# Kernel tuning notes

Measured on AMD Instinct MI355X. Metric: run time of the kernel, lower is better.

## Reference

```python
import jax, jax.numpy as jnp
import numpy as np

B, S, K, F = 256, 512, 32, 64
H1, H2 = 512, 256


def setup_inputs() -> dict:
    key = jax.random.key(0)
    ks = jax.random.split(key, 8)
    x = jax.random.normal(ks[0], (B, S, F), dtype=jnp.float32)
    neighborhood = jax.random.randint(ks[1], (S, K), 0, S)
    distances = jax.random.uniform(ks[2], (S, K), dtype=jnp.float32)
    in_w = K * (F + 1)  # 2080
    W1 = jax.random.normal(ks[3], (in_w, H1), dtype=jnp.float32) * 0.02
    b1 = jnp.zeros((H1,), dtype=jnp.float32)
    W2 = jax.random.normal(ks[4], (H1, H2), dtype=jnp.float32) * 0.02
    b2 = jnp.zeros((H2,), dtype=jnp.float32)
    Wd = jax.random.normal(ks[5], (H2, 1), dtype=jnp.float32) * 0.02
    bd = jnp.zeros((1,), dtype=jnp.float32)
    return {"x": x, "neighborhood": neighborhood, "distances": distances,
            "W1": W1, "b1": b1, "W2": W2, "b2": b2, "Wd": Wd, "bd": bd}


def reference(x, neighborhood, distances, W1, b1, W2, b2, Wd, bd):
    b, s, f = x.shape
    k = neighborhood.shape[1]
    # make_k_tensor: gather neighbors and append per-edge distance
    gathered = x[:, neighborhood, :]                      # [B, S, K, F]
    dist = jnp.broadcast_to(distances[None, :, :, None], (b, s, k, 1))
    kt = jnp.concatenate([gathered, dist], axis=-1)        # [B, S, K, F+1]
    # filter phase: shared MLP over flattened neighborhoods
    flat = kt.reshape(b * s, k * (f + 1))                  # [B*S, K*(F+1)]
    h = jax.nn.relu(flat @ W1 + b1)
    h = h @ W2 + b2                                        # [B*S, H2]
    h = h.reshape(b, s, -1)
    # max pool over sequence, then final dense
    m = jnp.max(h, axis=1)                                 # [B, H2]
    out = jax.nn.relu(m) @ Wd + bd                         # [B, 1]
    return out.squeeze(1)                                  # [B]
```

## Files before the change

kernel.cpp:

```cpp
#include <hip/hip_runtime.h>

typedef __attribute__((ext_vector_type(8))) short short8;
typedef __attribute__((ext_vector_type(4))) float f32x4;

constexpr int Bb = 256, Ss = 512, Kk = 32, Ff = 64, H1 = 512, H2 = 256;
constexpr int Mtot = Bb * Ss;
constexpr int KD1 = Kk * Ff;

#define DEVI static __device__ __forceinline__

DEVI unsigned short f2b(float f) {
  unsigned u = __float_as_uint(f);
  return (unsigned short)((u + 0x7FFFu + ((u >> 16) & 1u)) >> 16);
}

DEVI void stage16(const void* g, void* l) {
  __builtin_amdgcn_global_load_lds((const __attribute__((address_space(1))) void*)g,
                                   (__attribute__((address_space(3))) void*)l, 16, 0, 0);
}

__global__ void k_cvt_x(const float* __restrict__ x, unsigned short* __restrict__ xbf) {
  int i = blockIdx.x * 256 + threadIdx.x;
  float4 v = ((const float4*)x)[i];
  ushort4 o;
  o.x = f2b(v.x); o.y = f2b(v.y); o.z = f2b(v.z); o.w = f2b(v.w);
  ((ushort4*)xbf)[i] = o;
}

__global__ void k_w1t(const float* __restrict__ W1, unsigned short* __restrict__ w1t) {
  int idx = blockIdx.x * 256 + threadIdx.x;
  int h = idx >> 11, i = idx & 2047;
  int k = i >> 6, f = i & 63;
  w1t[idx] = f2b(W1[(k * 65 + f) * 512 + h]);
}

__global__ void k_w2t(const float* __restrict__ W2, unsigned short* __restrict__ w2t) {
  int idx = blockIdx.x * 256 + threadIdx.x;
  int n = idx >> 9, k = idx & 511;
  w2t[idx] = f2b(W2[k * 256 + n]);
}

__global__ void k_dbias(const float* __restrict__ W1, const float* __restrict__ b1,
                        const float* __restrict__ dist, float* __restrict__ dbias) {
  int idx = blockIdx.x * 256 + threadIdx.x;
  int s = idx >> 9, h = idx & 511;
  float a = b1[h];
  #pragma unroll
  for (int k = 0; k < 32; ++k)
    a += dist[s * 32 + k] * W1[(k * 65 + 64) * 512 + h];
  dbias[idx] = a;
}

__global__ __launch_bounds__(256, 2) void k_gemm1(
    const unsigned short* __restrict__ xbf, const unsigned short* __restrict__ w1t,
    const int* __restrict__ nb, const float* __restrict__ dbias,
    unsigned short* __restrict__ h1) {
  __shared__ __align__(16) unsigned short As[128 * 64];
  __shared__ __align__(16) unsigned short Bs[128 * 64];
  const int tid = threadIdx.x;
  const int lane = tid & 63;
  const int w = tid >> 6;
  const int wm = w >> 1, wn = w & 1;
  const int mblk = blockIdx.x >> 2;
  const int nblk = blockIdx.x & 3;
  const int r0 = mblk << 7;
  const int b = r0 >> 9;
  const int s0 = r0 & 511;
  const int ncol0 = nblk << 7;
  const int arow = lane >> 3;
  const int acol = (lane & 7) << 3;

  f32x4 acc[4][4];
  #pragma unroll
  for (int m = 0; m < 4; ++m)
    #pragma unroll
    for (int n = 0; n < 4; ++n) acc[m][n] = (f32x4){0.f, 0.f, 0.f, 0.f};

  for (int t = 0; t < 32; ++t) {
    #pragma unroll
    for (int i = 0; i < 4; ++i) {
      int rr = (w << 5) + (i << 3);
      int row = rr + arow;
      int j = nb[((s0 + row) << 5) + t];
      stage16(xbf + (((size_t)((b << 9) + j)) << 6) + acol, As + rr * 64);
    }
    #pragma unroll
    for (int i = 0; i < 4; ++i) {
      int rr = (w << 5) + (i << 3);
      int row = rr + arow;
      stage16(w1t + (((size_t)(ncol0 + row)) << 11) + (t << 6) + acol, Bs + rr * 64);
    }
    __syncthreads();
    #pragma unroll
    for (int ks = 0; ks < 2; ++ks) {
      short8 af[4], bfr[4];
      #pragma unroll
      for (int m = 0; m < 4; ++m)
        af[m] = *(const short8*)(As + ((wm << 6) + (m << 4) + (lane & 15)) * 64 + (ks << 5) + ((lane >> 4) << 3));
      #pragma unroll
      for (int n = 0; n < 4; ++n)
        bfr[n] = *(const short8*)(Bs + ((wn << 6) + (n << 4) + (lane & 15)) * 64 + (ks << 5) + ((lane >> 4) << 3));
      #pragma unroll
      for (int m = 0; m < 4; ++m)
        #pragma unroll
        for (int n = 0; n < 4; ++n)
          acc[m][n] = __builtin_amdgcn_mfma_f32_16x16x32_bf16(af[m], bfr[n], acc[m][n], 0, 0, 0);
    }
    __syncthreads();
  }

  #pragma unroll
  for (int m = 0; m < 4; ++m) {
    int rowl = (wm << 6) + (m << 4) + ((lane >> 4) << 2);
    #pragma unroll
    for (int n = 0; n < 4; ++n) {
      int col = ncol0 + (wn << 6) + (n << 4) + (lane & 15);
      #pragma unroll
      for (int r = 0; r < 4; ++r) {
        int row = r0 + rowl + r;
        float v = acc[m][n][r] + dbias[((row & 511) << 9) + col];
        v = v > 0.f ? v : 0.f;
        h1[((size_t)row << 9) + col] = f2b(v);
      }
    }
  }
}

__global__ __launch_bounds__(256, 2) void k_gemm2(
    const unsigned short* __restrict__ h1, const unsigned short* __restrict__ w2t,
    const float* __restrict__ b2, unsigned* __restrict__ mrelu) {
  __shared__ __align__(16) unsigned short As[128 * 64];
  __shared__ __align__(16) unsigned short Bs[128 * 64];
  const int tid = threadIdx.x;
  const int lane = tid & 63;
  const int w = tid >> 6;
  const int wm = w >> 1, wn = w & 1;
  const int mblk = blockIdx.x >> 1;
  const int nblk = blockIdx.x & 1;
  const int r0 = mblk << 7;
  const int b = r0 >> 9;
  const int ncol0 = nblk << 7;
  const int arow = lane >> 3;
  const int acol = (lane & 7) << 3;

  f32x4 acc[4][4];
  #pragma unroll
  for (int m = 0; m < 4; ++m)
    #pragma unroll
    for (int n = 0; n < 4; ++n) acc[m][n] = (f32x4){0.f, 0.f, 0.f, 0.f};

  for (int t = 0; t < 8; ++t) {
    #pragma unroll
    for (int i = 0; i < 4; ++i) {
      int rr = (w << 5) + (i << 3);
      int row = rr + arow;
      stage16(h1 + (((size_t)(r0 + row)) << 9) + (t << 6) + acol, As + rr * 64);
      stage16(w2t + (((size_t)(ncol0 + row)) << 9) + (t << 6) + acol, Bs + rr * 64);
    }
    __syncthreads();
    #pragma unroll
    for (int ks = 0; ks < 2; ++ks) {
      short8 af[4], bfr[4];
      #pragma unroll
      for (int m = 0; m < 4; ++m)
        af[m] = *(const short8*)(As + ((wm << 6) + (m << 4) + (lane & 15)) * 64 + (ks << 5) + ((lane >> 4) << 3));
      #pragma unroll
      for (int n = 0; n < 4; ++n)
        bfr[n] = *(const short8*)(Bs + ((wn << 6) + (n << 4) + (lane & 15)) * 64 + (ks << 5) + ((lane >> 4) << 3));
      #pragma unroll
      for (int m = 0; m < 4; ++m)
        #pragma unroll
        for (int n = 0; n < 4; ++n)
          acc[m][n] = __builtin_amdgcn_mfma_f32_16x16x32_bf16(af[m], bfr[n], acc[m][n], 0, 0, 0);
    }
    __syncthreads();
  }

  #pragma unroll
  for (int n = 0; n < 4; ++n) {
    int col = ncol0 + (wn << 6) + (n << 4) + (lane & 15);
    float cm = -1e30f;
    #pragma unroll
    for (int m = 0; m < 4; ++m)
      #pragma unroll
      for (int r = 0; r < 4; ++r) cm = fmaxf(cm, acc[m][n][r]);
    cm = fmaxf(cm, __shfl_xor(cm, 16));
    cm = fmaxf(cm, __shfl_xor(cm, 32));
    if ((lane >> 4) == 0) {
      float v = fmaxf(cm + b2[col], 0.f);
      atomicMax(mrelu + ((b << 8) + col), __float_as_uint(v));
    }
  }
}

__global__ void k_final(const unsigned* __restrict__ mrelu, const float* __restrict__ wd,
                        const float* __restrict__ bd, float* __restrict__ out) {
  int b = blockIdx.x, t = threadIdx.x;
  float v = __uint_as_float(mrelu[(b << 8) + t]) * wd[t];
  #pragma unroll
  for (int o = 32; o > 0; o >>= 1) v += __shfl_down(v, o);
  __shared__ float p[4];
  if ((t & 63) == 0) p[t >> 6] = v;
  __syncthreads();
  if (t == 0) out[b] = p[0] + p[1] + p[2] + p[3] + bd[0];
}

extern "C" void kernel_launch(void* const* d_in, const int* in_sizes, int n_in,
                              void* d_out, int out_size, void* d_ws, size_t ws_size,
                              hipStream_t stream) {
  (void)in_sizes; (void)n_in; (void)out_size; (void)ws_size;
  const float* x    = (const float*)d_in[0];
  const int*   nb   = (const int*)d_in[1];
  const float* dist = (const float*)d_in[2];
  const float* W1   = (const float*)d_in[3];
  const float* b1   = (const float*)d_in[4];
  const float* W2   = (const float*)d_in[5];
  const float* b2   = (const float*)d_in[6];
  const float* Wd   = (const float*)d_in[7];
  const float* bd   = (const float*)d_in[8];
  float* out = (float*)d_out;

  char* p = (char*)d_ws;
  unsigned short* xbf   = (unsigned short*)p; p += (size_t)Bb * Ss * Ff * 2;
  unsigned short* w1t   = (unsigned short*)p; p += (size_t)H1 * KD1 * 2;
  unsigned short* w2t   = (unsigned short*)p; p += (size_t)H2 * H1 * 2;
  float*          dbias = (float*)p;          p += (size_t)Ss * H1 * 4;
  unsigned*       mrelu = (unsigned*)p;       p += (size_t)Bb * H2 * 4;
  unsigned short* h1    = (unsigned short*)p; p += (size_t)Mtot * H1 * 2;

  hipMemsetAsync(mrelu, 0, (size_t)Bb * H2 * 4, stream);
  k_cvt_x<<<(Bb * Ss * Ff / 4) / 256, 256, 0, stream>>>(x, xbf);
  k_w1t<<<(H1 * KD1) / 256, 256, 0, stream>>>(W1, w1t);
  k_w2t<<<(H2 * H1) / 256, 256, 0, stream>>>(W2, w2t);
  k_dbias<<<(Ss * H1) / 256, 256, 0, stream>>>(W1, b1, dist, dbias);
  k_gemm1<<<(Mtot / 128) * (H1 / 128), 256, 0, stream>>>(xbf, w1t, nb, dbias, h1);
  k_gemm2<<<(Mtot / 128) * (H2 / 128), 256, 0, stream>>>(h1, w2t, b2, mrelu);
  k_final<<<Bb, 256, 0, stream>>>(mrelu, Wd, bd, out);
}
```

Measured before the change: 463.6 us.

## Swizzle LDS tiles and split GEMM chain into halves for L2-resident h1

Applies an XOR swizzle to the global-to-LDS staging column and the matching MFMA fragment reads in both GEMMs, so LDS reads should hit fewer bank conflicts. It adds an explicit vmcnt(0) wait before the barrier so the async LDS loads are complete before use. It also splits the batch rows into two halves, running gemm1 then gemm2 per half with a half-sized h1 buffer. This keeps the intermediate smaller and more likely to stay in cache, at the cost of extra launches and smaller grids per launch.

```diff
diff --git a/kernel.cpp b/kernel.cpp
--- a/kernel.cpp
+++ b/kernel.cpp
@@ -5,6 +5,7 @@
 
 constexpr int Bb = 256, Ss = 512, Kk = 32, Ff = 64, H1 = 512, H2 = 256;
 constexpr int Mtot = Bb * Ss;
+constexpr int Mh = Mtot / 2;
 constexpr int KD1 = Kk * Ff;
 
 #define DEVI static __device__ __forceinline__
@@ -51,10 +52,11 @@
   dbias[idx] = a;
 }
 
+
 __global__ __launch_bounds__(256, 2) void k_gemm1(
     const unsigned short* __restrict__ xbf, const unsigned short* __restrict__ w1t,
     const int* __restrict__ nb, const float* __restrict__ dbias,
-    unsigned short* __restrict__ h1) {
+    unsigned short* __restrict__ h1, int mbase) {
   __shared__ __align__(16) unsigned short As[128 * 64];
   __shared__ __align__(16) unsigned short Bs[128 * 64];
   const int tid = threadIdx.x;
@@ -63,12 +65,13 @@
   const int wm = w >> 1, wn = w & 1;
   const int mblk = blockIdx.x >> 2;
   const int nblk = blockIdx.x & 3;
-  const int r0 = mblk << 7;
-  const int b = r0 >> 9;
-  const int s0 = r0 & 511;
+  const int r0l = mblk << 7;
+  const int r0g = mbase + r0l;
+  const int b = r0g >> 9;
+  const int s0 = r0g & 511;
   const int ncol0 = nblk << 7;
   const int arow = lane >> 3;
-  const int acol = (lane & 7) << 3;
+  const int scol = (((lane & 7) ^ (lane >> 3)) << 3);
 
   f32x4 acc[4][4];
   #pragma unroll
@@ -82,24 +85,26 @@
       int rr = (w << 5) + (i << 3);
       int row = rr + arow;
       int j = nb[((s0 + row) << 5) + t];
-      stage16(xbf + (((size_t)((b << 9) + j)) << 6) + acol, As + rr * 64);
+      stage16(xbf + (((size_t)((b << 9) + j)) << 6) + scol, As + rr * 64);
     }
     #pragma unroll
     for (int i = 0; i < 4; ++i) {
       int rr = (w << 5) + (i << 3);
       int row = rr + arow;
-      stage16(w1t + (((size_t)(ncol0 + row)) << 11) + (t << 6) + acol, Bs + rr * 64);
-    }
+      stage16(w1t + (((size_t)(ncol0 + row)) << 11) + (t << 6) + scol, Bs + rr * 64);
+    }
+    asm volatile("s_waitcnt vmcnt(0)" ::: "memory");
     __syncthreads();
     #pragma unroll
     for (int ks = 0; ks < 2; ++ks) {
+      const int rdoff = ((((ks << 2) + (lane >> 4)) ^ (lane & 7)) << 3);
       short8 af[4], bfr[4];
       #pragma unroll
       for (int m = 0; m < 4; ++m)
-        af[m] = *(const short8*)(As + ((wm << 6) + (m << 4) + (lane & 15)) * 64 + (ks << 5) + ((lane >> 4) << 3));
+        af[m] = *(const short8*)(As + ((wm << 6) + (m << 4) + (lane & 15)) * 64 + rdoff);
       #pragma unroll
       for (int n = 0; n < 4; ++n)
-        bfr[n] = *(const short8*)(Bs + ((wn << 6) + (n << 4) + (lane & 15)) * 64 + (ks << 5) + ((lane >> 4) << 3));
+        bfr[n] = *(const short8*)(Bs + ((wn << 6) + (n << 4) + (lane & 15)) * 64 + rdoff);
       #pragma unroll
       for (int m = 0; m < 4; ++m)
         #pragma unroll
@@ -117,10 +122,10 @@
       int col = ncol0 + (wn << 6) + (n << 4) + (lane & 15);
       #pragma unroll
       for (int r = 0; r < 4; ++r) {
-        int row = r0 + rowl + r;
-        float v = acc[m][n][r] + dbias[((row & 511) << 9) + col];
+        int rowL = r0l + rowl + r;
+        float v = acc[m][n][r] + dbias[(((r0g + rowl + r) & 511) << 9) + col];
         v = v > 0.f ? v : 0.f;
-        h1[((size_t)row << 9) + col] = f2b(v);
+        h1[((size_t)rowL << 9) + col] = f2b(v);
       }
     }
   }
@@ -128,7 +133,7 @@
 
 __global__ __launch_bounds__(256, 2) void k_gemm2(
     const unsigned short* __restrict__ h1, const unsigned short* __restrict__ w2t,
-    const float* __restrict__ b2, unsigned* __restrict__ mrelu) {
+    const float* __restrict__ b2, unsigned* __restrict__ mrelu, int mbase) {
   __shared__ __align__(16) unsigned short As[128 * 64];
   __shared__ __align__(16) unsigned short Bs[128 * 64];
   const int tid = threadIdx.x;
@@ -137,11 +142,11 @@
   const int wm = w >> 1, wn = w & 1;
   const int mblk = blockIdx.x >> 1;
   const int nblk = blockIdx.x & 1;
-  const int r0 = mblk << 7;
-  const int b = r0 >> 9;
+  const int r0l = mblk << 7;
+  const int b = (mbase + r0l) >> 9;
   const int ncol0 = nblk << 7;
   const int arow = lane >> 3;
-  const int acol = (lane & 7) << 3;
+  const int scol = (((lane & 7) ^ (lane >> 3)) << 3);
 
   f32x4 acc[4][4];
   #pragma unroll
@@ -154,19 +159,21 @@
     for (int i = 0; i < 4; ++i) {
       int rr = (w << 5) + (i << 3);
       int row = rr + arow;
-      stage16(h1 + (((size_t)(r0 + row)) << 9) + (t << 6) + acol, As + rr * 64);
-      stage16(w2t + (((size_t)(ncol0 + row)) << 9) + (t << 6) + acol, Bs + rr * 64);
-    }
+      stage16(h1 + (((size_t)(r0l + row)) << 9) + (t << 6) + scol, As + rr * 64);
+      stage16(w2t + (((size_t)(ncol0 + row)) << 9) + (t << 6) + scol, Bs + rr * 64);
+    }
+    asm volatile("s_waitcnt vmcnt(0)" ::: "memory");
     __syncthreads();
     #pragma unroll
     for (int ks = 0; ks < 2; ++ks) {
+      const int rdoff = ((((ks << 2) + (lane >> 4)) ^ (lane & 7)) << 3);
       short8 af[4], bfr[4];
       #pragma unroll
       for (int m = 0; m < 4; ++m)
-        af[m] = *(const short8*)(As + ((wm << 6) + (m << 4) + (lane & 15)) * 64 + (ks << 5) + ((lane >> 4) << 3));
+        af[m] = *(const short8*)(As + ((wm << 6) + (m << 4) + (lane & 15)) * 64 + rdoff);
       #pragma unroll
       for (int n = 0; n < 4; ++n)
-        bfr[n] = *(const short8*)(Bs + ((wn << 6) + (n << 4) + (lane & 15)) * 64 + (ks << 5) + ((lane >> 4) << 3));
+        bfr[n] = *(const short8*)(Bs + ((wn << 6) + (n << 4) + (lane & 15)) * 64 + rdoff);
       #pragma unroll
       for (int m = 0; m < 4; ++m)
         #pragma unroll
@@ -226,14 +233,17 @@
   unsigned short* w2t   = (unsigned short*)p; p += (size_t)H2 * H1 * 2;
   float*          dbias = (float*)p;          p += (size_t)Ss * H1 * 4;
   unsigned*       mrelu = (unsigned*)p;       p += (size_t)Bb * H2 * 4;
-  unsigned short* h1    = (unsigned short*)p; p += (size_t)Mtot * H1 * 2;
+  unsigned short* h1    = (unsigned short*)p; p += (size_t)Mh * H1 * 2;
 
   hipMemsetAsync(mrelu, 0, (size_t)Bb * H2 * 4, stream);
   k_cvt_x<<<(Bb * Ss * Ff / 4) / 256, 256, 0, stream>>>(x, xbf);
   k_w1t<<<(H1 * KD1) / 256, 256, 0, stream>>>(W1, w1t);
   k_w2t<<<(H2 * H1) / 256, 256, 0, stream>>>(W2, w2t);
   k_dbias<<<(Ss * H1) / 256, 256, 0, stream>>>(W1, b1, dist, dbias);
-  k_gemm1<<<(Mtot / 128) * (H1 / 128), 256, 0, stream>>>(xbf, w1t, nb, dbias, h1);
-  k_gemm2<<<(Mtot / 128) * (H2 / 128), 256, 0, stream>>>(h1, w2t, b2, mrelu);
+  for (int hh = 0; hh < 2; ++hh) {
+    int mbase = hh * Mh;
+    k_gemm1<<<(Mh / 128) * (H1 / 128), 256, 0, stream>>>(xbf, w1t, nb, dbias, h1, mbase);
+    k_gemm2<<<(Mh / 128) * (H2 / 128), 256, 0, stream>>>(h1, w2t, b2, mrelu, mbase);
+  }
   k_final<<<Bb, 256, 0, stream>>>(mrelu, Wd, bd, out);
 }
```

Measured after the change: 442.8 us. 4.5% less time.

## Fuse both MLP GEMMs into one kernel keeping h1 in LDS

Applied to the files above, without the earlier changes.

Merges gemm1 and gemm2 into one kernel in which each 512-thread block computes a 128-row by full-512-column h1 tile and keeps it in LDS as bf16, then runs the second GEMM and max-pool from there. This removes the h1 round trip through global memory. The distance feature is folded in as an extra K window (bf16 distances times W1 distance rows) in place of the precomputed fp32 dbias table. The K loop uses a three-slot LDS ring with global_load_lds prefetch, swizzled LDS layouts and raw vmcnt/barrier control. The trade-off is one block per CU with 144KB of LDS, lower occupancy, and bf16 rounding of the distances.

```diff
diff --git a/kernel.cpp b/kernel.cpp
--- a/kernel.cpp
+++ b/kernel.cpp
@@ -4,10 +4,11 @@
 typedef __attribute__((ext_vector_type(4))) float f32x4;
 
 constexpr int Bb = 256, Ss = 512, Kk = 32, Ff = 64, H1 = 512, H2 = 256;
-constexpr int Mtot = Bb * Ss;
-constexpr int KD1 = Kk * Ff;
+constexpr int KD1E = 2080;
 
 #define DEVI static __device__ __forceinline__
+#define BARRIER asm volatile("s_barrier" ::: "memory")
+#define VMCNT(N) asm volatile("s_waitcnt vmcnt(" #N ")" ::: "memory")
 
 DEVI unsigned short f2b(float f) {
   unsigned u = __float_as_uint(f);
@@ -27,11 +28,20 @@
   ((ushort4*)xbf)[i] = o;
 }
 
+__global__ void k_cvt_dist(const float* __restrict__ dist, unsigned short* __restrict__ distbf) {
+  int i = blockIdx.x * 256 + threadIdx.x;
+  float4 v = ((const float4*)dist)[i];
+  ushort4 o;
+  o.x = f2b(v.x); o.y = f2b(v.y); o.z = f2b(v.z); o.w = f2b(v.w);
+  ((ushort4*)distbf)[i] = o;
+}
+
 __global__ void k_w1t(const float* __restrict__ W1, unsigned short* __restrict__ w1t) {
-  int idx = blockIdx.x * 256 + threadIdx.x;
-  int h = idx >> 11, i = idx & 2047;
-  int k = i >> 6, f = i & 63;
-  w1t[idx] = f2b(W1[(k * 65 + f) * 512 + h]);
+  int h = blockIdx.x;
+  for (int k = threadIdx.x; k < KD1E; k += 256) {
+    int row = (k < 2048) ? ((k >> 6) * 65 + (k & 63)) : ((k - 2048) * 65 + 64);
+    w1t[h * KD1E + k] = f2b(W1[row * 512 + h]);
+  }
 }
 
 __global__ void k_w2t(const float* __restrict__ W2, unsigned short* __restrict__ w2t) {
@@ -40,150 +50,145 @@
   w2t[idx] = f2b(W2[k * 256 + n]);
 }
 
-__global__ void k_dbias(const float* __restrict__ W1, const float* __restrict__ b1,
-                        const float* __restrict__ dist, float* __restrict__ dbias) {
-  int idx = blockIdx.x * 256 + threadIdx.x;
-  int s = idx >> 9, h = idx & 511;
-  float a = b1[h];
-  #pragma unroll
-  for (int k = 0; k < 32; ++k)
-    a += dist[s * 32 + k] * W1[(k * 65 + 64) * 512 + h];
-  dbias[idx] = a;
-}
-
-__global__ __launch_bounds__(256, 2) void k_gemm1(
+__global__ __launch_bounds__(512, 1) void k_fused(
     const unsigned short* __restrict__ xbf, const unsigned short* __restrict__ w1t,
-    const int* __restrict__ nb, const float* __restrict__ dbias,
-    unsigned short* __restrict__ h1) {
-  __shared__ __align__(16) unsigned short As[128 * 64];
-  __shared__ __align__(16) unsigned short Bs[128 * 64];
+    const int* __restrict__ nb, const unsigned short* __restrict__ distbf,
+    const float* __restrict__ b1, const unsigned short* __restrict__ w2t,
+    const float* __restrict__ b2, unsigned* __restrict__ mrelu) {
+  __shared__ __align__(16) char smem[147456];
   const int tid = threadIdx.x;
   const int lane = tid & 63;
   const int w = tid >> 6;
-  const int wm = w >> 1, wn = w & 1;
-  const int mblk = blockIdx.x >> 2;
-  const int nblk = blockIdx.x & 3;
-  const int r0 = mblk << 7;
-  const int b = r0 >> 9;
-  const int s0 = r0 & 511;
-  const int ncol0 = nblk << 7;
-  const int arow = lane >> 3;
-  const int acol = (lane & 7) << 3;
-
-  f32x4 acc[4][4];
+  const int wm = w >> 2, wn = w & 3;
+  const int b = blockIdx.x >> 2;
+  const int s0 = (blockIdx.x & 3) << 7;
+
+  const int arow = tid >> 2;
+  const int aCs = (((tid & 3) ^ ((tid >> 2) & 3)) << 3);
+  const int nbB = (s0 + arow) << 5;
+  const int rB = ((lane & 15) << 6) + ((((lane >> 4) ^ (lane & 3))) << 4);
+
+  f32x4 acc[4][8];
   #pragma unroll
   for (int m = 0; m < 4; ++m)
     #pragma unroll
-    for (int n = 0; n < 4; ++n) acc[m][n] = (f32x4){0.f, 0.f, 0.f, 0.f};
-
-  for (int t = 0; t < 32; ++t) {
-    #pragma unroll
-    for (int i = 0; i < 4; ++i) {
-      int rr = (w << 5) + (i << 3);
-      int row = rr + arow;
-      int j = nb[((s0 + row) << 5) + t];
-      stage16(xbf + (((size_t)((b << 9) + j)) << 6) + acol, As + rr * 64);
-    }
-    #pragma unroll
-    for (int i = 0; i < 4; ++i) {
-      int rr = (w << 5) + (i << 3);
-      int row = rr + arow;
-      stage16(w1t + (((size_t)(ncol0 + row)) << 11) + (t << 6) + acol, Bs + rr * 64);
-    }
-    __syncthreads();
-    #pragma unroll
-    for (int ks = 0; ks < 2; ++ks) {
-      short8 af[4], bfr[4];
-      #pragma unroll
-      for (int m = 0; m < 4; ++m)
-        af[m] = *(const short8*)(As + ((wm << 6) + (m << 4) + (lane & 15)) * 64 + (ks << 5) + ((lane >> 4) << 3));
+    for (int n = 0; n < 8; ++n) acc[m][n] = (f32x4){0.f, 0.f, 0.f, 0.f};
+
+#define STAGE_WIN(WIN, SLOT, JR)                                                  \
+  {                                                                               \
+    const int HS = ((WIN) < 64) ? (WIN) : 64;                                     \
+    char* sl = smem + (SLOT) * 40960;                                             \
+    if (HS < 64) {                                                                \
+      stage16(xbf + ((size_t)(((b << 9) + (JR)) << 6) + ((HS & 1) << 5) + aCs),   \
+              sl + (tid << 4));                                                   \
+    } else {                                                                      \
+      stage16(distbf + (((s0 + arow) << 5) + aCs), sl + (tid << 4));              \
+    }                                                                             \
+    const unsigned short* bbp = w1t + (HS << 5) + aCs;                            \
+    stage16(bbp + (size_t)(arow)       * KD1E, sl + 8192 + (tid << 4));           \
+    stage16(bbp + (size_t)(arow + 128) * KD1E, sl + 16384 + (tid << 4));          \
+    stage16(bbp + (size_t)(arow + 256) * KD1E, sl + 24576 + (tid << 4));          \
+    stage16(bbp + (size_t)(arow + 384) * KD1E, sl + 32768 + (tid << 4));          \
+  }
+
+  int j01 = nb[nbB];
+  int jreg = nb[nbB + 1];
+  STAGE_WIN(0, 0, j01);
+  STAGE_WIN(1, 1, j01);
+  VMCNT(0);
+
+  int csl = 0, psl = 2;
+  #pragma unroll 1
+  for (int W = 0; W < 65; ++W) {
+    BARRIER;
+    int jn = nb[nbB + (((W + 3) >> 1) < 32 ? ((W + 3) >> 1) : 31)];
+    const char* sl = smem + csl * 40960;
+    short8 af[4], bf[8];
+    #pragma unroll
+    for (int m = 0; m < 4; ++m)
+      af[m] = *(const short8*)(sl + (wm << 12) + (m << 10) + rB);
+    #pragma unroll
+    for (int n = 0; n < 8; ++n)
+      bf[n] = *(const short8*)(sl + 8192 + (wn << 13) + (n << 10) + rB);
+    STAGE_WIN(W + 2, psl, jreg);
+    VMCNT(6);
+    __builtin_amdgcn_s_setprio(1);
+    #pragma unroll
+    for (int m = 0; m < 4; ++m)
+      #pragma unroll
+      for (int n = 0; n < 8; ++n)
+        acc[m][n] = __builtin_amdgcn_mfma_f32_16x16x32_bf16(af[m], bf[n], acc[m][n], 0, 0, 0);
+    __builtin_amdgcn_s_setprio(0);
+    jreg = jn;
+    csl = (csl == 2) ? 0 : csl + 1;
+    psl = (psl == 2) ? 0 : psl + 1;
+  }
+#undef STAGE_WIN
+  VMCNT(0);
+  BARRIER;
+
+  {
+    float b1v[8];
+    #pragma unroll
+    for (int n = 0; n < 8; ++n) b1v[n] = b1[(wn << 7) + (n << 4) + (lane & 15)];
+    #pragma unroll
+    for (int m = 0; m < 4; ++m) {
+      #pragma unroll
+      for (int n = 0; n < 8; ++n) {
+        const int col = (wn << 7) + (n << 4) + (lane & 15);
+        #pragma unroll
+        for (int r = 0; r < 4; ++r) {
+          const int row = (wm << 6) + (m << 4) + ((lane >> 4) << 2) + r;
+          float v = acc[m][n][r] + b1v[n];
+          v = v > 0.f ? v : 0.f;
+          unsigned off = (unsigned)(((row << 10) + (col << 1)) ^ ((row & 7) << 4));
+          *(unsigned short*)(smem + off) = f2b(v);
+        }
+      }
+    }
+  }
+  BARRIER;
+
+  f32x4 acc2[4][4];
+  #pragma unroll
+  for (int m = 0; m < 4; ++m)
+    #pragma unroll
+    for (int n = 0; n < 4; ++n) acc2[m][n] = (f32x4){0.f, 0.f, 0.f, 0.f};
+
+  for (int kc = 0; kc < 16; ++kc) {
+    {
+      const unsigned short* src = w2t + (kc << 5) + aCs;
+      stage16(src + (size_t)(arow) * 512,       smem + 131072 + (tid << 4));
+      stage16(src + (size_t)(arow + 128) * 512, smem + 139264 + (tid << 4));
+    }
+    VMCNT(0);
+    BARRIER;
+    short8 a2[4], b2f[4];
+    #pragma unroll
+    for (int m = 0; m < 4; ++m) {
+      const int row = (wm << 6) + (m << 4) + (lane & 15);
+      a2[m] = *(const short8*)(smem + ((((row << 10) + (kc << 6) + ((lane >> 4) << 4))
+                                       ^ ((lane & 7) << 4))));
+    }
+    #pragma unroll
+    for (int n = 0; n < 4; ++n)
+      b2f[n] = *(const short8*)(smem + 131072 + (wn << 12) + (n << 10) + rB);
+    #pragma unroll
+    for (int m = 0; m < 4; ++m)
       #pragma unroll
       for (int n = 0; n < 4; ++n)
-        bfr[n] = *(const short8*)(Bs + ((wn << 6) + (n << 4) + (lane & 15)) * 64 + (ks << 5) + ((lane >> 4) << 3));
-      #pragma unroll
-      for (int m = 0; m < 4; ++m)
-        #pragma unroll
-        for (int n = 0; n < 4; ++n)
-          acc[m][n] = __builtin_amdgcn_mfma_f32_16x16x32_bf16(af[m], bfr[n], acc[m][n], 0, 0, 0);
-    }
-    __syncthreads();
-  }
-
-  #pragma unroll
-  for (int m = 0; m < 4; ++m) {
-    int rowl = (wm << 6) + (m << 4) + ((lane >> 4) << 2);
-    #pragma unroll
-    for (int n = 0; n < 4; ++n) {
-      int col = ncol0 + (wn << 6) + (n << 4) + (lane & 15);
-      #pragma unroll
-      for (int r = 0; r < 4; ++r) {
-        int row = r0 + rowl + r;
-        float v = acc[m][n][r] + dbias[((row & 511) << 9) + col];
-        v = v > 0.f ? v : 0.f;
-        h1[((size_t)row << 9) + col] = f2b(v);
-      }
-    }
-  }
-}
-
-__global__ __launch_bounds__(256, 2) void k_gemm2(
-    const unsigned short* __restrict__ h1, const unsigned short* __restrict__ w2t,
-    const float* __restrict__ b2, unsigned* __restrict__ mrelu) {
-  __shared__ __align__(16) unsigned short As[128 * 64];
-  __shared__ __align__(16) unsigned short Bs[128 * 64];
-  const int tid = threadIdx.x;
-  const int lane = tid & 63;
-  const int w = tid >> 6;
-  const int wm = w >> 1, wn = w & 1;
-  const int mblk = blockIdx.x >> 1;
-  const int nblk = blockIdx.x & 1;
-  const int r0 = mblk << 7;
-  const int b = r0 >> 9;
-  const int ncol0 = nblk << 7;
-  const int arow = lane >> 3;
-  const int acol = (lane & 7) << 3;
-
-  f32x4 acc[4][4];
-  #pragma unroll
-  for (int m = 0; m < 4; ++m)
-    #pragma unroll
-    for (int n = 0; n < 4; ++n) acc[m][n] = (f32x4){0.f, 0.f, 0.f, 0.f};
-
-  for (int t = 0; t < 8; ++t) {
-    #pragma unroll
-    for (int i = 0; i < 4; ++i) {
-      int rr = (w << 5) + (i << 3);
-      int row = rr + arow;
-      stage16(h1 + (((size_t)(r0 + row)) << 9) + (t << 6) + acol, As + rr * 64);
-      stage16(w2t + (((size_t)(ncol0 + row)) << 9) + (t << 6) + acol, Bs + rr * 64);
-    }
-    __syncthreads();
-    #pragma unroll
-    for (int ks = 0; ks < 2; ++ks) {
-      short8 af[4], bfr[4];
-      #pragma unroll
-      for (int m = 0; m < 4; ++m)
-        af[m] = *(const short8*)(As + ((wm << 6) + (m << 4) + (lane & 15)) * 64 + (ks << 5) + ((lane >> 4) << 3));
-      #pragma unroll
-      for (int n = 0; n < 4; ++n)
-        bfr[n] = *(const short8*)(Bs + ((wn << 6) + (n << 4) + (lane & 15)) * 64 + (ks << 5) + ((lane >> 4) << 3));
-      #pragma unroll
-      for (int m = 0; m < 4; ++m)
-        #pragma unroll
-        for (int n = 0; n < 4; ++n)
-          acc[m][n] = __builtin_amdgcn_mfma_f32_16x16x32_bf16(af[m], bfr[n], acc[m][n], 0, 0, 0);
-    }
-    __syncthreads();
+        acc2[m][n] = __builtin_amdgcn_mfma_f32_16x16x32_bf16(a2[m], b2f[n], acc2[m][n], 0, 0, 0);
+    BARRIER;
   }
 
   #pragma unroll
   for (int n = 0; n < 4; ++n) {
-    int col = ncol0 + (wn << 6) + (n << 4) + (lane & 15);
+    const int col = (wn << 6) + (n << 4) + (lane & 15);
     float cm = -1e30f;
     #pragma unroll
     for (int m = 0; m < 4; ++m)
       #pragma unroll
-      for (int r = 0; r < 4; ++r) cm = fmaxf(cm, acc[m][n][r]);
+      for (int r = 0; r < 4; ++r) cm = fmaxf(cm, acc2[m][n][r]);
     cm = fmaxf(cm, __shfl_xor(cm, 16));
     cm = fmaxf(cm, __shfl_xor(cm, 32));
     if ((lane >> 4) == 0) {
@@ -221,19 +226,17 @@
   float* out = (float*)d_out;
 
   char* p = (char*)d_ws;
-  unsigned short* xbf   = (unsigned short*)p; p += (size_t)Bb * Ss * Ff * 2;
-  unsigned short* w1t   = (unsigned short*)p; p += (size_t)H1 * KD1 * 2;
-  unsigned short* w2t   = (unsigned short*)p; p += (size_t)H2 * H1 * 2;
-  float*          dbias = (float*)p;          p += (size_t)Ss * H1 * 4;
-  unsigned*       mrelu = (unsigned*)p;       p += (size_t)Bb * H2 * 4;
-  unsigned short* h1    = (unsigned short*)p; p += (size_t)Mtot * H1 * 2;
+  unsigned short* xbf    = (unsigned short*)p; p += (size_t)Bb * Ss * Ff * 2;
+  unsigned short* w1t    = (unsigned short*)p; p += (size_t)H1 * KD1E * 2;
+  unsigned short* w2t    = (unsigned short*)p; p += (size_t)H2 * H1 * 2;
+  unsigned short* distbf = (unsigned short*)p; p += (size_t)Ss * Kk * 2;
+  unsigned*       mrelu  = (unsigned*)p;       p += (size_t)Bb * H2 * 4;
 
   hipMemsetAsync(mrelu, 0, (size_t)Bb * H2 * 4, stream);
   k_cvt_x<<<(Bb * Ss * Ff / 4) / 256, 256, 0, stream>>>(x, xbf);
-  k_w1t<<<(H1 * KD1) / 256, 256, 0, stream>>>(W1, w1t);
+  k_cvt_dist<<<(Ss * Kk / 4) / 256, 256, 0, stream>>>(dist, distbf);
+  k_w1t<<<H1, 256, 0, stream>>>(W1, w1t);
   k_w2t<<<(H2 * H1) / 256, 256, 0, stream>>>(W2, w2t);
-  k_dbias<<<(Ss * H1) / 256, 256, 0, stream>>>(W1, b1, dist, dbias);
-  k_gemm1<<<(Mtot / 128) * (H1 / 128), 256, 0, stream>>>(xbf, w1t, nb, dbias, h1);
-  k_gemm2<<<(Mtot / 128) * (H2 / 128), 256, 0, stream>>>(h1, w2t, b2, mrelu);
+  k_fused<<<Bb * 4, 512, 0, stream>>>(xbf, w1t, nb, distbf, b1, w2t, b2, mrelu);
   k_final<<<Bb, 256, 0, stream>>>(mrelu, Wd, bd, out);
 }
```

Result: faster. 450.7 us (-2.8%).
